# Kernel optimization log

Measured on AMD Instinct MI355X. Metric: run time of the kernel, lower is better.

Reference implementation:

```python
import jax, jax.numpy as jnp
import numpy as np

B, T, K = 256, 512, 128

def setup_inputs() -> dict:
    key = jax.random.key(0)
    k1, k2, k3, k4, k5 = jax.random.split(key, 5)
    emissions = jax.random.normal(k1, (B, T, K), dtype=jnp.float32)
    tags = jax.random.randint(k2, (B, T), 0, K)
    mask = jnp.ones((B, T), dtype=bool)
    # xavier_uniform_ for trans: limit = sqrt(6/(fan_in+fan_out))
    limit = float(np.sqrt(6.0 / (K + K)))
    trans = jax.random.uniform(k3, (K, K), minval=-limit, maxval=limit, dtype=jnp.float32)
    start = 0.1 * jax.random.normal(k4, (K,), dtype=jnp.float32)
    end = 0.1 * jax.random.normal(k5, (K,), dtype=jnp.float32)
    return {"emissions": emissions, "trans": trans, "start": start, "end": end,
            "tags": tags, "mask": mask}

def reference(emissions, trans, start, end, tags, mask):
    # --- log partition (forward algorithm) via lax.scan over time ---
    em_t = jnp.moveaxis(emissions, 1, 0)  # [T,B,K]
    mk_t = jnp.moveaxis(mask, 1, 0)       # [T,B]
    alpha0 = start + em_t[0]              # [B,K]

    def step(alpha, xs):
        em, mk = xs                                      # em:[B,K], mk:[B]
        scores = alpha[:, :, None] + trans[None] + em[:, None, :]  # [B,K,K]
        alpha_next = jax.nn.logsumexp(scores, axis=1)    # [B,K]
        alpha = jnp.where(mk[:, None], alpha_next, alpha)
        return alpha, None

    alpha, _ = jax.lax.scan(step, alpha0, (em_t[1:], mk_t[1:]))
    logZ = jax.nn.logsumexp(alpha + end, axis=1)  # [B]

    # --- gold path score, fully vectorized ---
    emit = jnp.take_along_axis(emissions, tags[..., None], axis=2)[..., 0]  # [B,T]
    trans_sc = trans[tags[:, :-1], tags[:, 1:]]                             # [B,T-1]
    step_sc = (emit[:, 1:] + trans_sc) * mask[:, 1:]                        # masked steps
    score = start[tags[:, 0]] + emit[:, 0] + jnp.sum(step_sc, axis=1)
    last_idx = jnp.sum(mask, axis=1).astype(jnp.int32) - 1
    last_tags = jnp.take_along_axis(tags, last_idx[:, None], axis=1)[:, 0]
    score = score + end[last_tags]

    return jnp.mean(logZ - score)
```

## Files before the change

### kernel.cpp

```cpp
#include <hip/hip_runtime.h>

#define B_ 256
#define T_ 512
#define K_ 128
#define HALF_T 256

typedef _Float16 half8 __attribute__((ext_vector_type(8)));
typedef _Float16 half2_t __attribute__((ext_vector_type(2)));
typedef float f32x4 __attribute__((ext_vector_type(4)));

__device__ inline float fast_exp2(float x) {
#if __has_builtin(__builtin_amdgcn_exp2f)
    return __builtin_amdgcn_exp2f(x);
#else
    return exp2f(x);
#endif
}
__device__ inline float fast_log2(float x) {
#if __has_builtin(__builtin_amdgcn_logf)
    return __builtin_amdgcn_logf(x);
#else
    return log2f(x);
#endif
}
__device__ inline float dot2(half2_t a, half2_t b, float c) {
#if __has_builtin(__builtin_amdgcn_fdot2)
    return __builtin_amdgcn_fdot2(a, b, c, false);
#else
    return fmaf((float)a.x, (float)b.x, fmaf((float)a.y, (float)b.y, c));
#endif
}
__device__ inline unsigned pack2(float x, float y) {
#if __has_builtin(__builtin_amdgcn_cvt_pkrtz)
    auto h = __builtin_amdgcn_cvt_pkrtz(x, y);
    return __builtin_bit_cast(unsigned, h);
#else
    half2_t h; h.x = (_Float16)x; h.y = (_Float16)y;
    return __builtin_bit_cast(unsigned, h);
#endif
}
__device__ inline half2_t as_h2(unsigned u) {
    return __builtin_bit_cast(half2_t, u);
}

#define WS_TT   0
#define WS_FV   (K_ * K_)
#define WS_BV   (WS_FV + B_ * 64)
#define WS_M2F  (WS_BV + B_ * 64)
#define WS_M2B  (WS_M2F + B_)
#define WS_SC   (WS_M2B + B_)

__global__ void crf_transpose_kernel(const float* __restrict__ trans,
                                     float* __restrict__ transT)
{
    int idx = blockIdx.x * 256 + threadIdx.x;
    int r = idx >> 7, c = idx & (K_ - 1);
    transT[c * K_ + r] = trans[r * K_ + c];
}


__global__ __launch_bounds__(256, 1)
void crf_half_kernel(const float* __restrict__ emissions,
                     const float* __restrict__ trans,
                     const float* __restrict__ start,
                     const float* __restrict__ endv,
                     const int* __restrict__ tags,
                     unsigned* __restrict__ ws_u32)
{
    const int bid  = blockIdx.x;
    const bool fwd = bid < (B_ / 2);
    const int bp   = fwd ? bid : bid - (B_ / 2);
    const int b0g  = bp * 2;
    const int tid  = threadIdx.x;
    const int wave = tid >> 6;
    const int lane = tid & 63;
    const int l15  = lane & 15;
    const int g4   = lane >> 4;
    const int colbase = (wave << 5) + l15;

    __shared__ __align__(16) _Float16 emlds[2][HALF_T][K_];
    __shared__ __align__(16) _Float16 aebuf[2][2][160];
    __shared__ float wred[4];

    const float* transT = (const float*)(ws_u32 + WS_TT);
    unsigned*    fv     = ws_u32 + WS_FV;
    unsigned*    bv     = ws_u32 + WS_BV;
    float*       m2f    = (float*)(ws_u32 + WS_M2F);
    float*       m2b    = (float*)(ws_u32 + WS_M2B);
    float*       scp    = (float*)(ws_u32 + WS_SC);

    const float L  = 1.44269504f;
    const float C2 = 7.7f;
    const float LN2 = 0.69314718f;

    const float* M   = fwd ? trans : transT;
    const float* sv_ = fwd ? start : endv;
    const int rbase  = fwd ? 0 : HALF_T;
    const int r0     = fwd ? 0 : (HALF_T - 1);
    const int NIT    = fwd ? (HALF_T - 1) : HALF_T;
    const int em_base = fwd ? 0 : (HALF_T - 1);
    const int em_sign = fwd ? 1 : -1;

    for (int b = 0; b < 2; ++b) {
        const float4* ef4 = reinterpret_cast<const float4*>(
            emissions + ((size_t)(b0g + b) * T_ + rbase) * K_);
        for (int it = 0; it < 32; ++it) {
            int f = it * 256 + tid;
            float4 v = ef4[f];
            int r = f >> 5, m = f & 31;
            uint2 w;
            w.x = pack2(v.x, v.y);
            w.y = pack2(v.z, v.w);
            *reinterpret_cast<uint2*>(&emlds[b][r][4 * m]) = w;
        }
    }

#define EFRAG(kc, nc, dst)                                                  \
    {                                                                       \
        half8 t;                                                            \
        _Pragma("unroll")                                                   \
        for (int i = 0; i < 8; ++i) {                                       \
            int k = (kc) * 32 + g4 * 8 + i;                                 \
            t[i] = (_Float16)fast_exp2(M[k * K_ + colbase + 16 * (nc)] * L);\
        }                                                                   \
        dst = t;                                                            \
    }
    half8 e00, e01, e10, e11, e20, e21, e30, e31;
    EFRAG(0, 0, e00) EFRAG(0, 1, e01)
    EFRAG(1, 0, e10) EFRAG(1, 1, e11)
    EFRAG(2, 0, e20) EFRAG(2, 1, e21)
    EFRAG(3, 0, e30) EFRAG(3, 1, e31)
#undef EFRAG

    __syncthreads();

    {
        int ib = tid >> 7, ij = tid & 127;
        float z = (sv_[ij] + (float)emlds[ib][r0][ij]) * L;
        float mx = z;
        #pragma unroll
        for (int d = 1; d < 64; d <<= 1) mx = fmaxf(mx, __shfl_xor(mx, d));
        if (lane == 0) wred[wave] = mx;
    }
    __syncthreads();
    float M2_0 = fmaxf(wred[0], wred[1]);
    float M2_1 = fmaxf(wred[2], wred[3]);
    {
        int ib = tid >> 7, ij = tid & 127;
        float Mz = ib == 0 ? M2_0 : M2_1;
        float z = (sv_[ij] + (float)emlds[ib][r0][ij]) * L;
        aebuf[0][ib][ij] = (_Float16)fast_exp2(z - Mz);
    }
    __syncthreads();

    const int bsel = lane & 1;
    for (int n = 1; n <= NIT; ++n) {
        const _Float16* aerow = &aebuf[(n - 1) & 1][0][0];

        const char* abase = (const char*)aerow + bsel * 320 + (g4 << 4);
        half8 a0 = *reinterpret_cast<const half8*>(abase);
        half8 a1 = *reinterpret_cast<const half8*>(abase + 64);
        half8 a2 = *reinterpret_cast<const half8*>(abase + 128);
        half8 a3 = *reinterpret_cast<const half8*>(abase + 192);

        uint2 p0 = *reinterpret_cast<const uint2*>(aerow);
        uint2 p1 = *reinterpret_cast<const uint2*>(aerow + 160);

        const int emrow = em_base + em_sign * n;
        float em00 = 0.f, em01 = 0.f, em10 = 0.f, em11 = 0.f;
        if (emrow >= 0) {
            em00 = (float)emlds[0][emrow][colbase];
            em01 = (float)emlds[0][emrow][colbase + 16];
            em10 = (float)emlds[1][emrow][colbase];
            em11 = (float)emlds[1][emrow][colbase + 16];
        }

        f32x4 acc0 = {0.f, 0.f, 0.f, 0.f};
        f32x4 acc1 = {0.f, 0.f, 0.f, 0.f};
        acc0 = __builtin_amdgcn_mfma_f32_16x16x32_f16(a0, e00, acc0, 0, 0, 0);
        acc1 = __builtin_amdgcn_mfma_f32_16x16x32_f16(a0, e01, acc1, 0, 0, 0);
        acc0 = __builtin_amdgcn_mfma_f32_16x16x32_f16(a1, e10, acc0, 0, 0, 0);
        acc1 = __builtin_amdgcn_mfma_f32_16x16x32_f16(a1, e11, acc1, 0, 0, 0);
        acc0 = __builtin_amdgcn_mfma_f32_16x16x32_f16(a2, e20, acc0, 0, 0, 0);
        acc1 = __builtin_amdgcn_mfma_f32_16x16x32_f16(a2, e21, acc1, 0, 0, 0);
        acc0 = __builtin_amdgcn_mfma_f32_16x16x32_f16(a3, e30, acc0, 0, 0, 0);
        acc1 = __builtin_amdgcn_mfma_f32_16x16x32_f16(a3, e31, acc1, 0, 0, 0);

        half2_t q0 = as_h2(p0.x), q1 = as_h2(p0.y);
        float pm0 = fmaxf(fmaxf((float)q0.x, (float)q0.y),
                          fmaxf((float)q1.x, (float)q1.y));
        half2_t r0h = as_h2(p1.x), r1h = as_h2(p1.y);
        float pm1 = fmaxf(fmaxf((float)r0h.x, (float)r0h.y),
                          fmaxf((float)r1h.x, (float)r1h.y));
        pm0 = fmaxf(pm0, 6.1e-5f);
        pm1 = fmaxf(pm1, 6.1e-5f);
        float corr0 = fast_log2(pm0);
        float corr1 = fast_log2(pm1);

        float F00 = fast_exp2(fmaf(em00, L, -C2 - corr0));
        float F01 = fast_exp2(fmaf(em01, L, -C2 - corr0));
        float F10 = fast_exp2(fmaf(em10, L, -C2 - corr1));
        float F11 = fast_exp2(fmaf(em11, L, -C2 - corr1));

        if (g4 == 0) {
            _Float16* nb = &aebuf[n & 1][0][0];
            nb[colbase]            = (_Float16)(acc0[0] * F00);
            nb[colbase + 16]       = (_Float16)(acc1[0] * F01);
            nb[160 + colbase]      = (_Float16)(acc0[1] * F10);
            nb[160 + colbase + 16] = (_Float16)(acc1[1] * F11);
        }
        M2_0 += C2 + corr0;
        M2_1 += C2 + corr1;
        __syncthreads();
    }

    {
        int ib = tid >> 7, ij = tid & 127;
        _Float16 v = aebuf[NIT & 1][ib][ij];
        unsigned short* dst = (unsigned short*)(fwd ? fv : bv);
        dst[(size_t)(b0g + ib) * 128 + ij] = __builtin_bit_cast(unsigned short, v);
    }
    if (tid == 0) {
        (fwd ? m2f : m2b)[b0g]     = M2_0;
        (fwd ? m2f : m2b)[b0g + 1] = M2_1;
    }

    if (fwd) {
        for (int bi = 0; bi < 2; ++bi) {
            const int*   tg = tags + (size_t)(b0g + bi) * T_;
            const float* eb = emissions + (size_t)(b0g + bi) * T_ * K_;
            float sc = 0.0f;
            for (int k = tid; k < T_; k += 256) {
                int cur = tg[k];
                sc += eb[(size_t)k * K_ + cur];
                if (k > 0) sc += trans[tg[k - 1] * K_ + cur];
            }
            #pragma unroll
            for (int d = 1; d < 64; d <<= 1) sc += __shfl_xor(sc, d);
            __syncthreads();
            if (lane == 0) wred[wave] = sc;
            __syncthreads();
            if (tid == 0)
                scp[b0g + bi] = wred[0] + wred[1] + wred[2] + wred[3]
                              + start[tg[0]] + endv[tg[T_ - 1]];
        }
    }
}

__global__ void crf_join_kernel(const unsigned* __restrict__ ws_u32,
                                float* __restrict__ out)
{
    const unsigned* fv  = ws_u32 + WS_FV;
    const unsigned* bv  = ws_u32 + WS_BV;
    const float*    m2f = (const float*)(ws_u32 + WS_M2F);
    const float*    m2b = (const float*)(ws_u32 + WS_M2B);
    const float*    scp = (const float*)(ws_u32 + WS_SC);

    const float LN2 = 0.69314718f;
    int b = threadIdx.x;

    float acc = 0.0f;
    #pragma unroll
    for (int k = 0; k < 64; ++k)
        acc = dot2(as_h2(fv[b * 64 + k]), as_h2(bv[b * 64 + k]), acc);

    float logZ = (m2f[b] + m2b[b] + fast_log2(acc)) * LN2;
    float v = logZ - scp[b];

    #pragma unroll
    for (int d = 1; d < 64; d <<= 1) v += __shfl_xor(v, d);
    __shared__ float w[4];
    if ((threadIdx.x & 63) == 0) w[threadIdx.x >> 6] = v;
    __syncthreads();
    if (threadIdx.x == 0)
        out[0] = (w[0] + w[1] + w[2] + w[3]) * (1.0f / 256.0f);
}

extern "C" void kernel_launch(void* const* d_in, const int* in_sizes, int n_in,
                              void* d_out, int out_size, void* d_ws, size_t ws_size,
                              hipStream_t stream)
{
    const float* emissions = (const float*)d_in[0];
    const float* trans     = (const float*)d_in[1];
    const float* start     = (const float*)d_in[2];
    const float* endv      = (const float*)d_in[3];
    const int*   tags      = (const int*)d_in[4];

    unsigned* ws = (unsigned*)d_ws;

    crf_transpose_kernel<<<K_ * K_ / 256, 256, 0, stream>>>(trans, (float*)(ws + WS_TT));
    crf_half_kernel<<<B_, 256, 0, stream>>>(emissions, trans, start, endv, tags, ws);
    crf_join_kernel<<<1, 256, 0, stream>>>(ws, (float*)d_out);
}
```

Measured before the change: 114.1 us.

## Split gold-path scoring across halves, batch emission loads, split MFMA accumulators

Gold path scoring used to run only in the forward-half blocks. It is now split so each half-block scores its own 256 timesteps, and the join kernel sums the two partial scores. The emission prefetch into LDS now issues 16 float4 loads before converting and storing them, which raises memory-level parallelism. The MFMA chain also uses two independent accumulators per output to shorten the dependency chain in the serial recurrence. The costs are higher register pressure and a small amount of extra workspace.

```diff
diff --git a/kernel.cpp b/kernel.cpp
--- a/kernel.cpp
+++ b/kernel.cpp
@@ -48,7 +48,8 @@
 #define WS_BV   (WS_FV + B_ * 64)
 #define WS_M2F  (WS_BV + B_ * 64)
 #define WS_M2B  (WS_M2F + B_)
-#define WS_SC   (WS_M2B + B_)
+#define WS_SCF  (WS_M2B + B_)
+#define WS_SCB  (WS_SCF + B_)
 
 __global__ void crf_transpose_kernel(const float* __restrict__ trans,
                                      float* __restrict__ transT)
@@ -87,11 +88,11 @@
     unsigned*    bv     = ws_u32 + WS_BV;
     float*       m2f    = (float*)(ws_u32 + WS_M2F);
     float*       m2b    = (float*)(ws_u32 + WS_M2B);
-    float*       scp    = (float*)(ws_u32 + WS_SC);
+    float*       scf    = (float*)(ws_u32 + WS_SCF);
+    float*       scb    = (float*)(ws_u32 + WS_SCB);
 
     const float L  = 1.44269504f;
     const float C2 = 7.7f;
-    const float LN2 = 0.69314718f;
 
     const float* M   = fwd ? trans : transT;
     const float* sv_ = fwd ? start : endv;
@@ -101,17 +102,29 @@
     const int em_base = fwd ? 0 : (HALF_T - 1);
     const int em_sign = fwd ? 1 : -1;
 
-    for (int b = 0; b < 2; ++b) {
-        const float4* ef4 = reinterpret_cast<const float4*>(
-            emissions + ((size_t)(b0g + b) * T_ + rbase) * K_);
-        for (int it = 0; it < 32; ++it) {
-            int f = it * 256 + tid;
-            float4 v = ef4[f];
-            int r = f >> 5, m = f & 31;
-            uint2 w;
-            w.x = pack2(v.x, v.y);
-            w.y = pack2(v.z, v.w);
-            *reinterpret_cast<uint2*>(&emlds[b][r][4 * m]) = w;
+    {
+        const float4* ef4_0 = reinterpret_cast<const float4*>(
+            emissions + ((size_t)b0g * T_ + rbase) * K_);
+        const float4* ef4_1 = reinterpret_cast<const float4*>(
+            emissions + ((size_t)(b0g + 1) * T_ + rbase) * K_);
+        #pragma unroll
+        for (int rd = 0; rd < 4; ++rd) {
+            const float4* src = (rd < 2) ? ef4_0 : ef4_1;
+            const int bsel2 = (rd < 2) ? 0 : 1;
+            const int base = (rd & 1) * 16;
+            float4 tmp[16];
+            #pragma unroll
+            for (int u = 0; u < 16; ++u)
+                tmp[u] = src[(base + u) * 256 + tid];
+            #pragma unroll
+            for (int u = 0; u < 16; ++u) {
+                int f = (base + u) * 256 + tid;
+                int r = f >> 5, m = f & 31;
+                uint2 w;
+                w.x = pack2(tmp[u].x, tmp[u].y);
+                w.y = pack2(tmp[u].z, tmp[u].w);
+                *reinterpret_cast<uint2*>(&emlds[bsel2][r][4 * m]) = w;
+            }
         }
     }
 
@@ -175,16 +188,18 @@
             em11 = (float)emlds[1][emrow][colbase + 16];
         }
 
-        f32x4 acc0 = {0.f, 0.f, 0.f, 0.f};
-        f32x4 acc1 = {0.f, 0.f, 0.f, 0.f};
-        acc0 = __builtin_amdgcn_mfma_f32_16x16x32_f16(a0, e00, acc0, 0, 0, 0);
-        acc1 = __builtin_amdgcn_mfma_f32_16x16x32_f16(a0, e01, acc1, 0, 0, 0);
-        acc0 = __builtin_amdgcn_mfma_f32_16x16x32_f16(a1, e10, acc0, 0, 0, 0);
-        acc1 = __builtin_amdgcn_mfma_f32_16x16x32_f16(a1, e11, acc1, 0, 0, 0);
-        acc0 = __builtin_amdgcn_mfma_f32_16x16x32_f16(a2, e20, acc0, 0, 0, 0);
-        acc1 = __builtin_amdgcn_mfma_f32_16x16x32_f16(a2, e21, acc1, 0, 0, 0);
-        acc0 = __builtin_amdgcn_mfma_f32_16x16x32_f16(a3, e30, acc0, 0, 0, 0);
-        acc1 = __builtin_amdgcn_mfma_f32_16x16x32_f16(a3, e31, acc1, 0, 0, 0);
+        f32x4 acc0a = {0.f, 0.f, 0.f, 0.f};
+        f32x4 acc0b = {0.f, 0.f, 0.f, 0.f};
+        f32x4 acc1a = {0.f, 0.f, 0.f, 0.f};
+        f32x4 acc1b = {0.f, 0.f, 0.f, 0.f};
+        acc0a = __builtin_amdgcn_mfma_f32_16x16x32_f16(a0, e00, acc0a, 0, 0, 0);
+        acc1a = __builtin_amdgcn_mfma_f32_16x16x32_f16(a0, e01, acc1a, 0, 0, 0);
+        acc0b = __builtin_amdgcn_mfma_f32_16x16x32_f16(a1, e10, acc0b, 0, 0, 0);
+        acc1b = __builtin_amdgcn_mfma_f32_16x16x32_f16(a1, e11, acc1b, 0, 0, 0);
+        acc0a = __builtin_amdgcn_mfma_f32_16x16x32_f16(a2, e20, acc0a, 0, 0, 0);
+        acc1a = __builtin_amdgcn_mfma_f32_16x16x32_f16(a2, e21, acc1a, 0, 0, 0);
+        acc0b = __builtin_amdgcn_mfma_f32_16x16x32_f16(a3, e30, acc0b, 0, 0, 0);
+        acc1b = __builtin_amdgcn_mfma_f32_16x16x32_f16(a3, e31, acc1b, 0, 0, 0);
 
         half2_t q0 = as_h2(p0.x), q1 = as_h2(p0.y);
         float pm0 = fmaxf(fmaxf((float)q0.x, (float)q0.y),
@@ -203,11 +218,15 @@
         float F11 = fast_exp2(fmaf(em11, L, -C2 - corr1));
 
         if (g4 == 0) {
+            float v00 = acc0a[0] + acc0b[0];
+            float v01 = acc1a[0] + acc1b[0];
+            float v10 = acc0a[1] + acc0b[1];
+            float v11 = acc1a[1] + acc1b[1];
             _Float16* nb = &aebuf[n & 1][0][0];
-            nb[colbase]            = (_Float16)(acc0[0] * F00);
-            nb[colbase + 16]       = (_Float16)(acc1[0] * F01);
-            nb[160 + colbase]      = (_Float16)(acc0[1] * F10);
-            nb[160 + colbase + 16] = (_Float16)(acc1[1] * F11);
+            nb[colbase]            = (_Float16)(v00 * F00);
+            nb[colbase + 16]       = (_Float16)(v01 * F01);
+            nb[160 + colbase]      = (_Float16)(v10 * F10);
+            nb[160 + colbase + 16] = (_Float16)(v11 * F11);
         }
         M2_0 += C2 + corr0;
         M2_1 += C2 + corr1;
@@ -225,24 +244,24 @@
         (fwd ? m2f : m2b)[b0g + 1] = M2_1;
     }
 
-    if (fwd) {
+    {
+        const int kk = (fwd ? 0 : HALF_T) + tid;
         for (int bi = 0; bi < 2; ++bi) {
             const int*   tg = tags + (size_t)(b0g + bi) * T_;
             const float* eb = emissions + (size_t)(b0g + bi) * T_ * K_;
-            float sc = 0.0f;
-            for (int k = tid; k < T_; k += 256) {
-                int cur = tg[k];
-                sc += eb[(size_t)k * K_ + cur];
-                if (k > 0) sc += trans[tg[k - 1] * K_ + cur];
-            }
+            int cur = tg[kk];
+            float sc = eb[(size_t)kk * K_ + cur];
+            if (kk > 0) sc += trans[tg[kk - 1] * K_ + cur];
+            if (fwd && kk == 0) sc += start[cur];
+            if (!fwd && kk == T_ - 1) sc += endv[cur];
             #pragma unroll
             for (int d = 1; d < 64; d <<= 1) sc += __shfl_xor(sc, d);
             __syncthreads();
             if (lane == 0) wred[wave] = sc;
             __syncthreads();
             if (tid == 0)
-                scp[b0g + bi] = wred[0] + wred[1] + wred[2] + wred[3]
-                              + start[tg[0]] + endv[tg[T_ - 1]];
+                (fwd ? scf : scb)[b0g + bi] =
+                    wred[0] + wred[1] + wred[2] + wred[3];
         }
     }
 }
@@ -254,7 +273,8 @@
     const unsigned* bv  = ws_u32 + WS_BV;
     const float*    m2f = (const float*)(ws_u32 + WS_M2F);
     const float*    m2b = (const float*)(ws_u32 + WS_M2B);
-    const float*    scp = (const float*)(ws_u32 + WS_SC);
+    const float*    scf = (const float*)(ws_u32 + WS_SCF);
+    const float*    scb = (const float*)(ws_u32 + WS_SCB);
 
     const float LN2 = 0.69314718f;
     int b = threadIdx.x;
@@ -265,7 +285,7 @@
         acc = dot2(as_h2(fv[b * 64 + k]), as_h2(bv[b * 64 + k]), acc);
 
     float logZ = (m2f[b] + m2b[b] + fast_log2(acc)) * LN2;
-    float v = logZ - scp[b];
+    float v = logZ - scf[b] - scb[b];
 
     #pragma unroll
     for (int d = 1; d < 64; d <<= 1) v += __shfl_xor(v, d);
```

After: 116.4 us. 2.0% more time.
